# Kernel tuning notes

Measured on AMD Instinct MI355X. Metric: run time of the kernel, lower is better.

The kernel has to match this reference:

```python
import jax, jax.numpy as jnp
import numpy as np

NHEAD = 8
TOP_K = 2


def layernorm(x, g, b, eps=1e-5):
    m = x.mean(-1, keepdims=True)
    v = x.var(-1, keepdims=True)
    return (x - m) * jax.lax.rsqrt(v + eps) * g + b


def causal_conv(x, w, b, dil):
    # x: [N, C, L], w: [O, I, K] (torch layout), left-pad for causality
    pad = (w.shape[-1] - 1) * dil
    y = jax.lax.conv_general_dilated(x, w, (1,), [(pad, 0)], rhs_dilation=(dil,),
                                     dimension_numbers=('NCH', 'OIH', 'NCH'))
    return y + b[None, :, None]


def sinusoidal_pe(L, d):
    pos = jnp.arange(L, dtype=jnp.float32)[:, None]
    div = jnp.exp(jnp.arange(0, d, 2, dtype=jnp.float32) * (-np.log(10000.0) / d))
    pe = jnp.zeros((L, d), jnp.float32)
    pe = pe.at[:, 0::2].set(jnp.sin(pos * div))
    pe = pe.at[:, 1::2].set(jnp.cos(pos * div))
    return pe


def _forward(x, sensor_mask, enc_proj_w, enc_proj_b, tcn_w1, tcn_b1, tcn_w2, tcn_b2,
             enc_norm_g, enc_norm_b, pool_proj_w, pool_proj_b, pos_inter,
             t_wq, t_bq, t_wk, t_bk, t_wv, t_bv, t_wo, t_bo,
             t_ln1_g, t_ln1_b, t_ln2_g, t_ln2_b,
             t_ff1_w, t_ff1_b, t_ff2_w, t_ff2_b, t_out_g, t_out_b,
             exp_w1, exp_b1, exp_w2, exp_b2,
             gate_f_w, gate_f_b, gate_fail_w, gate_fail_b, gate_rca_w, gate_rca_b,
             pred_w, pred_b, fail_w, fail_b, rca_w, rca_b):
    B, L, M = x.shape
    P = enc_proj_w.shape[1]
    D = pool_proj_w.shape[1]
    O = exp_w2.shape[-1]
    # mask sensors, grab last value per sensor (globally standardized)
    xm = jnp.transpose(x, (0, 2, 1)) * sensor_mask[:, :, None]        # [B, M, L]
    last_val = xm[:, :, -1]                                           # [B, M]
    seqs = xm.reshape(B * M, L, 1)
    # per-sensor TCN encoder
    h = seqs @ enc_proj_w + enc_proj_b                                # [BM, L, P]
    h = h + sinusoidal_pe(L, P)[None]
    h = jnp.transpose(h, (0, 2, 1))                                   # [BM, P, L]
    for i in range(tcn_w1.shape[0]):
        dil = 2 ** i
        out = jax.nn.relu(causal_conv(h, tcn_w1[i], tcn_b1[i], dil))
        out = jax.nn.relu(causal_conv(out, tcn_w2[i], tcn_b2[i], dil))
        h = jax.nn.relu(out + h)                                      # channels equal -> identity residual
    h = layernorm(jnp.transpose(h, (0, 2, 1)), enc_norm_g, enc_norm_b)  # [BM, L, T]
    feats = h.reshape(B, M, L, -1) * sensor_mask[:, :, None, None]
    pooled = feats.mean(axis=2)                                       # [B, M, T]
    t = pooled @ pool_proj_w + pool_proj_b                            # [B, M, D]
    # inter-sensor transformer (pre-LN), key padding mask where sensor_mask==0
    t = t + pos_inter[:, :M, :]
    bias = jnp.where(sensor_mask == 0, -1e9, 0.0)[:, None, None, :]   # [B,1,1,M]
    dh = D // NHEAD
    for l in range(t_wq.shape[0]):
        y = layernorm(t, t_ln1_g[l], t_ln1_b[l])
        q = (y @ t_wq[l] + t_bq[l]).reshape(B, M, NHEAD, dh)
        k = (y @ t_wk[l] + t_bk[l]).reshape(B, M, NHEAD, dh)
        v = (y @ t_wv[l] + t_bv[l]).reshape(B, M, NHEAD, dh)
        s = jnp.einsum('bqhd,bkhd->bhqk', q, k) / jnp.sqrt(jnp.float32(dh)) + bias
        a = jax.nn.softmax(s, axis=-1)
        o = jnp.einsum('bhqk,bkhd->bqhd', a, v).reshape(B, M, D) @ t_wo[l] + t_bo[l]
        t = t + o
        y2 = layernorm(t, t_ln2_g[l], t_ln2_b[l])
        t = t + jax.nn.relu(y2 @ t_ff1_w[l] + t_ff1_b[l]) @ t_ff2_w[l] + t_ff2_b[l]
    ctx = layernorm(t, t_out_g, t_out_b) * sensor_mask[:, :, None]    # [B, M, D]
    # global context: masked mean + masked max over valid sensors
    cnt = jnp.maximum(sensor_mask.sum(1, keepdims=True), 1.0)
    mean_ctx = ctx.sum(1) / cnt                                       # [B, D]
    max_ctx = jnp.where(sensor_mask[:, :, None] > 0, ctx, -1e9).max(1)
    g = jnp.concatenate([mean_ctx, max_ctx], -1)                      # [B, 2D]

    def moe(x_exp, gate_in, gw, gb):
        logits = gate_in @ gw + gb                                    # [N, E]
        vals, idx = jax.lax.top_k(logits, TOP_K)
        w = jax.nn.softmax(vals, -1)
        hh = jax.nn.relu(jnp.einsum('nd,edh->neh', x_exp, exp_w1) + exp_b1)
        allo = jnp.einsum('neh,eho->neo', hh, exp_w2) + exp_b2        # [N, E, O]
        sel = jnp.take_along_axis(allo, idx[..., None], axis=1)
        return (sel * w[..., None]).sum(1)                            # [N, O]

    y_f = moe(g, g, gate_f_w, gate_f_b)                               # [B, O]
    y_fail = moe(g, g, gate_fail_w, gate_fail_b)
    tok = ctx.reshape(B * M, D)
    exp_in_rca = jnp.concatenate(
        [tok, jnp.broadcast_to(mean_ctx[:, None, :], (B, M, D)).reshape(B * M, D)], -1)
    y_rca = moe(exp_in_rca, tok, gate_rca_w, gate_rca_b).reshape(B, M, O)
    # heads
    pred_in = jnp.concatenate([pooled, ctx, jnp.broadcast_to(y_f[:, None, :], (B, M, O))], -1)
    pred = pred_in @ pred_w + pred_b + last_val[..., None]            # [B, M, PH]
    fail_out = y_fail @ fail_w + fail_b                               # [B, FH]
    rca_in = jnp.concatenate([pooled, ctx, y_rca], -1)
    rca_out = (rca_in @ rca_w + rca_b)[..., 0]                        # [B, M]
    return jnp.concatenate([pred.reshape(B, -1), fail_out, rca_out], axis=1)


def setup_inputs() -> dict:
    key = jax.random.key(0)
    ks = iter(jax.random.split(key, 64))
    nrm = lambda shape, s=0.05: jax.random.normal(next(ks), shape, jnp.float32) * s
    B, L, M = 16, 512, 32
    P, T, D, E, EH, O = 64, 64, 128, 16, 512, 128
    NL, LEV, K = 2, 4, 3
    return dict(
        x=jax.random.normal(next(ks), (B, L, M), jnp.float32),
        sensor_mask=jax.random.randint(next(ks), (B, M), 0, 2).astype(jnp.float32),
        enc_proj_w=nrm((1, P)), enc_proj_b=jnp.zeros((P,)),
        tcn_w1=nrm((LEV, P, P, K)), tcn_b1=jnp.zeros((LEV, P)),
        tcn_w2=nrm((LEV, P, P, K)), tcn_b2=jnp.zeros((LEV, P)),
        enc_norm_g=jnp.ones((T,)), enc_norm_b=jnp.zeros((T,)),
        pool_proj_w=nrm((T, D)), pool_proj_b=jnp.zeros((D,)),
        pos_inter=nrm((1, M, D), 0.02),
        t_wq=nrm((NL, D, D)), t_bq=jnp.zeros((NL, D)),
        t_wk=nrm((NL, D, D)), t_bk=jnp.zeros((NL, D)),
        t_wv=nrm((NL, D, D)), t_bv=jnp.zeros((NL, D)),
        t_wo=nrm((NL, D, D)), t_bo=jnp.zeros((NL, D)),
        t_ln1_g=jnp.ones((NL, D)), t_ln1_b=jnp.zeros((NL, D)),
        t_ln2_g=jnp.ones((NL, D)), t_ln2_b=jnp.zeros((NL, D)),
        t_ff1_w=nrm((NL, D, 2 * D)), t_ff1_b=jnp.zeros((NL, 2 * D)),
        t_ff2_w=nrm((NL, 2 * D, D)), t_ff2_b=jnp.zeros((NL, D)),
        t_out_g=jnp.ones((D,)), t_out_b=jnp.zeros((D,)),
        exp_w1=nrm((E, 2 * D, EH)), exp_b1=jnp.zeros((E, EH)),
        exp_w2=nrm((E, EH, O)), exp_b2=jnp.zeros((E, O)),
        gate_f_w=nrm((2 * D, E)), gate_f_b=jnp.zeros((E,)),
        gate_fail_w=nrm((2 * D, E)), gate_fail_b=jnp.zeros((E,)),
        gate_rca_w=nrm((D, E)), gate_rca_b=jnp.zeros((E,)),
        pred_w=nrm((T + D + O, 3)), pred_b=jnp.zeros((3,)),
        fail_w=nrm((O, 3)), fail_b=jnp.zeros((3,)),
        rca_w=nrm((T + D + O, 1)), rca_b=jnp.zeros((1,)),
    )


def reference(x, sensor_mask, enc_proj_w, enc_proj_b, tcn_w1, tcn_b1, tcn_w2, tcn_b2,
              enc_norm_g, enc_norm_b, pool_proj_w, pool_proj_b, pos_inter,
              t_wq, t_bq, t_wk, t_bk, t_wv, t_bv, t_wo, t_bo,
              t_ln1_g, t_ln1_b, t_ln2_g, t_ln2_b,
              t_ff1_w, t_ff1_b, t_ff2_w, t_ff2_b, t_out_g, t_out_b,
              exp_w1, exp_b1, exp_w2, exp_b2,
              gate_f_w, gate_f_b, gate_fail_w, gate_fail_b, gate_rca_w, gate_rca_b,
              pred_w, pred_b, fail_w, fail_b, rca_w, rca_b):
    return _forward(x, sensor_mask, enc_proj_w, enc_proj_b, tcn_w1, tcn_b1, tcn_w2, tcn_b2,
                    enc_norm_g, enc_norm_b, pool_proj_w, pool_proj_b, pos_inter,
                    t_wq, t_bq, t_wk, t_bk, t_wv, t_bv, t_wo, t_bo,
                    t_ln1_g, t_ln1_b, t_ln2_g, t_ln2_b,
                    t_ff1_w, t_ff1_b, t_ff2_w, t_ff2_b, t_out_g, t_out_b,
                    exp_w1, exp_b1, exp_w2, exp_b2,
                    gate_f_w, gate_f_b, gate_fail_w, gate_fail_b, gate_rca_w, gate_rca_b,
                    pred_w, pred_b, fail_w, fail_b, rca_w, rca_b)
```

## Files before the change

### kernel.cpp

```cpp
#include <hip/hip_runtime.h>
#include <hip/hip_bf16.h>

#define B_   16
#define L_   512
#define M_   32
#define P_   64
#define D_   128
#define NH_  8
#define NL_  2
#define E_   16
#define EH_  512
#define O_   128

#define CH2   256
#define HALO  60
#define PADF  16
#define ROWS2 336
#define LDW   64

typedef short  bf16x8 __attribute__((ext_vector_type(8)));
typedef float  f32x4  __attribute__((ext_vector_type(4)));
typedef unsigned short us4 __attribute__((ext_vector_type(4)));
typedef unsigned short us8 __attribute__((ext_vector_type(8)));

__device__ __forceinline__ float bf2f(unsigned short h) {
  unsigned u = ((unsigned)h) << 16; float f; __builtin_memcpy(&f, &u, 4); return f;
}
__device__ __forceinline__ unsigned short f2bf(float f) {
  unsigned u; __builtin_memcpy(&u, &f, 4);
  u += 0x7fffu + ((u >> 16) & 1);
  return (unsigned short)(u >> 16);
}
__device__ __forceinline__ int swz(int row, int col_us) {
  return row * LDW + (col_us ^ ((row & 7) << 3));
}

#define XFW_PPW   0
#define XFW_QKVO  8192
#define XFW_F1    139264
#define XFW_F2    204800

__global__ __launch_bounds__(256) void prep_kernel(
    const float* __restrict__ ppw,
    const float* __restrict__ twq, const float* __restrict__ twk,
    const float* __restrict__ twv, const float* __restrict__ two,
    const float* __restrict__ f1w, const float* __restrict__ f2w,
    const float* __restrict__ ew1, const float* __restrict__ ew2,
    const float* __restrict__ tw1, const float* __restrict__ tw2,
    unsigned short* __restrict__ xfw, unsigned short* __restrict__ w1t,
    unsigned short* __restrict__ w2t, unsigned short* __restrict__ wpack,
    float* __restrict__ peT) {
  const int b = blockIdx.x;
  const int tid = threadIdx.x;
  if (b < 834) {
    __shared__ float tl[64][65];
    const float* src; unsigned short* dst; int R, C, tr, tc;
    if (b < 2) {
      src = ppw; dst = xfw + XFW_PPW; R = 64; C = 128; tr = 0; tc = b;
    } else if (b < 34) {
      int t = b - 2; int lg = t >> 2; int l = lg >> 2, gem = lg & 3;
      int tt = t & 3; tr = tt >> 1; tc = tt & 1;
      const float* s4 = (gem == 0) ? twq : (gem == 1) ? twk : (gem == 2) ? twv : two;
      src = s4 + l * 16384; dst = xfw + XFW_QKVO + l * 65536 + gem * 16384; R = 128; C = 128;
    } else if (b < 50) {
      int t = b - 34; int l = t >> 3; int tt = t & 7; tr = tt >> 2; tc = tt & 3;
      src = f1w + l * 32768; dst = xfw + XFW_F1 + l * 32768; R = 128; C = 256;
    } else if (b < 66) {
      int t = b - 50; int l = t >> 3; int tt = t & 7; tr = tt >> 1; tc = tt & 1;
      src = f2w + l * 32768; dst = xfw + XFW_F2 + l * 32768; R = 256; C = 128;
    } else if (b < 578) {
      int t = b - 66; int e = t >> 5; int tt = t & 31; tr = tt >> 3; tc = tt & 7;
      src = ew1 + e * 131072; dst = w1t + e * 131072; R = 256; C = 512;
    } else {
      int t = b - 578; int e = t >> 4; int tt = t & 15; tr = tt >> 1; tc = tt & 1;
      src = ew2 + e * 65536; dst = w2t + e * 65536; R = 512; C = 128;
    }
    for (int i = tid; i < 4096; i += 256) {
      int r = i >> 6, c = i & 63;
      tl[r][c] = src[(tr * 64 + r) * C + tc * 64 + c];
    }
    __syncthreads();
    for (int i = tid; i < 4096; i += 256) {
      int c = i >> 6, r = i & 63;
      dst[(tc * 64 + c) * R + tr * 64 + r] = f2bf(tl[r][c]);
    }
  } else if (b < 840) {
    int base = (b - 834) * 16384;
    for (int q = tid; q < 16384; q += 256) {
      int i = base + q;
      int c = i & 63, o = (i >> 6) & 63, tlc = i >> 12;
      int t = tlc % 3, lc = tlc / 3, lvl = lc >> 1;
      const float* src = (lc & 1) ? tw2 : tw1;
      wpack[i] = f2bf(src[lvl * 12288 + o * 192 + c * 3 + t]);
    }
  } else {
    int base = (b - 840) * 16384;
    for (int q = tid; q < 16384; q += 256) {
      int j = base + q; int ll = j >> 6, c = j & 63;
      float dv = expf(-0.14391157f * (float)(c & ~1));
      float ang = (float)ll * dv;
      peT[j] = (c & 1) ? cosf(ang) : sinf(ang);
    }
  }
}

template <int DIL, bool RES>
__device__ __forceinline__ void conv_mfma(const unsigned short* __restrict__ IN,
                                          unsigned short* __restrict__ OUT,
                                          const unsigned short* __restrict__ Wt,
                                          const float* __restrict__ bias, bool zh) {
  const int tid  = threadIdx.x;
  const int wid  = tid >> 6;
  const int lane = tid & 63;
  const int fr   = lane & 15;
  const int g    = lane >> 4;
  const int ot0  = (wid & 1) * 2;
  const int ng   = wid >> 1;

  bf16x8 Af[2][6];
#pragma unroll
  for (int oo = 0; oo < 2; ++oo)
#pragma unroll
    for (int t = 0; t < 3; ++t)
#pragma unroll
      for (int kh = 0; kh < 2; ++kh) {
        int wr = t * 64 + (ot0 + oo) * 16 + fr;
        Af[oo][t * 2 + kh] = *(const bf16x8*)(Wt + swz(wr, kh * 32 + g * 8));
      }
  float bv[2][4];
#pragma unroll
  for (int oo = 0; oo < 2; ++oo)
#pragma unroll
    for (int j = 0; j < 4; ++j) bv[oo][j] = bias[(ot0 + oo) * 16 + g * 4 + j];

#pragma unroll
  for (int k = 0; k < 3; ++k) {
    const int nt = ng + k * 8;
    if (nt < 20) {
      const int rb = PADF + nt * 16 + fr;
      bf16x8 Bf[6];
#pragma unroll
      for (int t = 0; t < 3; ++t) {
        int r = rb + (t - 2) * DIL;
#pragma unroll
        for (int kh = 0; kh < 2; ++kh)
          Bf[t * 2 + kh] = *(const bf16x8*)(IN + swz(r, kh * 32 + g * 8));
      }
      f32x4 acc[2];
#pragma unroll
      for (int oo = 0; oo < 2; ++oo) {
        f32x4 a; a[0] = bv[oo][0]; a[1] = bv[oo][1]; a[2] = bv[oo][2]; a[3] = bv[oo][3];
        acc[oo] = a;
      }
#pragma unroll
      for (int f = 0; f < 6; ++f)
#pragma unroll
        for (int oo = 0; oo < 2; ++oo)
          acc[oo] = __builtin_amdgcn_mfma_f32_16x16x32_bf16(Af[oo][f], Bf[f], acc[oo], 0, 0, 0);

      const float zm = (zh && rb < PADF + HALO) ? 0.f : 1.f;
#pragma unroll
      for (int oo = 0; oo < 2; ++oo) {
        unsigned short* op = OUT + swz(rb, (ot0 + oo) * 16 + g * 4);
        us4 old;
        if (RES) old = *(const us4*)op;
        us4 st;
#pragma unroll
        for (int j = 0; j < 4; ++j) {
          float v = fmaxf(acc[oo][j], 0.f);
          if (RES) v = fmaxf(v + bf2f(old[j]), 0.f);
          st[j] = f2bf(v * zm);
        }
        *(us4*)op = st;
      }
    }
  }
}

__global__ __launch_bounds__(1024) void tcn_kernel(
    const float* __restrict__ x, const float* __restrict__ mask,
    const float* __restrict__ pw, const float* __restrict__ pb,
    const unsigned short* __restrict__ wpack,
    const float* __restrict__ b1, const float* __restrict__ b2,
    const float* __restrict__ peT,
    const float* __restrict__ lng, const float* __restrict__ lnb,
    float* __restrict__ psum2) {
  extern __shared__ unsigned short smu[];
  unsigned short* A  = smu;
  unsigned short* Bq = A + ROWS2 * LDW;
  unsigned short* W0 = Bq + ROWS2 * LDW;
  unsigned short* W1 = W0 + 192 * LDW;
  float* fbase = (float*)(W1 + 192 * LDW);
  float* xr   = fbase;
  float* pwpb = fbase + 336;
  float* mst  = fbase;
  float* pp   = fbase + 512;

  const int bx = blockIdx.x;
  const int seq = bx & 511;
  const int chunk = bx >> 9;
  const int b = seq >> 5;
  const int m = seq & 31;
  if (mask[b * M_ + m] == 0.0f) return;
  const int tid = threadIdx.x;
  const bool zh = (chunk == 0);
  const int lbase = chunk * CH2 - HALO;

  float4 wreg[2];
#define WLOAD(li)                                                               \
  { wreg[0] = *(const float4*)(wpack + (li) * 12288 + (tid >> 3) * 64 + (tid & 7) * 8); \
    if (tid < 512)                                                              \
      wreg[1] = *(const float4*)(wpack + (li) * 12288 + ((tid >> 3) + 128) * 64 + (tid & 7) * 8); }
#define WSTORE(buf)                                                             \
  { *(float4*)((buf) + swz(tid >> 3, (tid & 7) * 8)) = wreg[0];                 \
    if (tid < 512)                                                              \
      *(float4*)((buf) + swz((tid >> 3) + 128, (tid & 7) * 8)) = wreg[1]; }

  WLOAD(0);
  if (tid < 64)       pwpb[tid] = pw[tid];
  else if (tid < 128) pwpb[tid] = pb[tid - 64];
  if (tid < ROWS2) {
    int w = tid - PADF, l = lbase + w;
    float xv = 0.f;
    if (w >= 0 && w < CH2 + HALO && l >= 0 && l < L_) xv = x[(b * L_ + l) * M_ + m];
    xr[tid] = xv;
  }
  __syncthreads();

  for (int idx = tid; idx < ROWS2 * 8; idx += 1024) {
    int r = idx >> 3, c0 = (idx & 7) * 8;
    int w = r - PADF, l = lbase + w;
    us8 st;
    if (w >= 0 && w < CH2 + HALO && l >= 0 && l < L_) {
      float xv = xr[r];
      const float4* pe4 = (const float4*)(peT + l * 64 + c0);
      float4 pa = pe4[0], pc = pe4[1];
      float pe[8] = {pa.x, pa.y, pa.z, pa.w, pc.x, pc.y, pc.z, pc.w};
#pragma unroll
      for (int j = 0; j < 8; ++j) {
        int c = c0 + j;
        st[j] = f2bf(fmaf(xv, pwpb[c], pwpb[64 + c]) + pe[j]);
      }
    } else {
#pragma unroll
      for (int j = 0; j < 8; ++j) st[j] = 0;
    }
    *(us8*)(A + swz(r, c0)) = st;
  }
  for (int idx = tid; idx < PADF * LDW; idx += 1024) Bq[idx] = 0;
  WSTORE(W0); WLOAD(1);
  __syncthreads();

  conv_mfma<1, false>(A, Bq, W0, b1 + 0,   zh); WSTORE(W1); WLOAD(2); __syncthreads();
  conv_mfma<1, true >(Bq, A, W1, b2 + 0,   zh); WSTORE(W0); WLOAD(3); __syncthreads();
  conv_mfma<2, false>(A, Bq, W0, b1 + 64,  zh); WSTORE(W1); WLOAD(4); __syncthreads();
  conv_mfma<2, true >(Bq, A, W1, b2 + 64,  zh); WSTORE(W0); WLOAD(5); __syncthreads();
  conv_mfma<4, false>(A, Bq, W0, b1 + 128, zh); WSTORE(W1); WLOAD(6); __syncthreads();
  conv_mfma<4, true >(Bq, A, W1, b2 + 128, zh); WSTORE(W0); WLOAD(7); __syncthreads();
  conv_mfma<8, false>(A, Bq, W0, b1 + 192, zh); WSTORE(W1);           __syncthreads();
  conv_mfma<8, true >(Bq, A, W1, b2 + 192, zh);                       __syncthreads();
#undef WLOAD
#undef WSTORE

  if (tid < CH2) {
    int r = PADF + HALO + tid;
    float s = 0.f, ss = 0.f;
#pragma unroll
    for (int c0 = 0; c0 < 64; c0 += 8) {
      bf16x8 vv = *(const bf16x8*)(A + swz(r, c0));
#pragma unroll
      for (int j = 0; j < 8; ++j) { float v = bf2f((unsigned short)vv[j]); s += v; ss += v * v; }
    }
    float mu = s * 0.015625f;
    float var = fmaxf(ss * 0.015625f - mu * mu, 0.0f);
    mst[tid] = mu;
    mst[CH2 + tid] = rsqrtf(var + 1e-5f);
  }
  __syncthreads();
  {
    int p = tid & 63, q = tid >> 6;
    float accp = 0.f;
    int r0 = PADF + HALO + q * 16;
    for (int r = r0; r < r0 + 16; ++r)
      accp += (bf2f(A[swz(r, p)]) - mst[r - PADF - HALO]) * mst[CH2 + r - PADF - HALO];
    pp[tid] = accp;
  }
  __syncthreads();
  if (tid < 64) {
    float acc = 0.f;
#pragma unroll
    for (int q = 0; q < 16; ++q) acc += pp[q * 64 + tid];
    psum2[chunk * 32768 + seq * 64 + tid] = lng[tid] * acc + 256.0f * lnb[tid];
  }
}

__device__ __forceinline__ void ln_sums(const float* __restrict__ In, float* mst, float* scr) {
  const int t = threadIdx.x;
  if (t < 256) {
    int mm = t >> 3, sg = t & 7;
    const float* ip = In + mm * 132 + sg * 16;
    float s = 0, ss = 0;
#pragma unroll
    for (int j = 0; j < 16; ++j) { float v = ip[j]; s += v; ss += v * v; }
    scr[t] = s; scr[256 + t] = ss;
  }
  __syncthreads();
  if (t < 32) {
    float s = 0, ss = 0;
#pragma unroll
    for (int k = 0; k < 8; ++k) { s += scr[t * 8 + k]; ss += scr[256 + t * 8 + k]; }
    float mu = s * 0.0078125f;
    float var = fmaxf(ss * 0.0078125f - mu * mu, 0.f);
    mst[t] = mu;
    mst[32 + t] = rsqrtf(var + 1e-5f);
  }
  __syncthreads();
}

__device__ __forceinline__ void ln_bf(const float* __restrict__ In, unsigned short* __restrict__ Out,
                                      const float* __restrict__ g, const float* __restrict__ b,
                                      float* mst, float* scr) {
  ln_sums(In, mst, scr);
  for (int idx = threadIdx.x; idx < 4096; idx += 512) {
    int mm = idx >> 7, j = idx & 127;
    Out[mm * 136 + j] = f2bf((In[mm * 132 + j] - mst[mm]) * mst[32 + mm] * g[j] + b[j]);
  }
  __syncthreads();
}

__device__ __forceinline__ void ln_f32(const float* __restrict__ In, float* __restrict__ Out,
                                       const float* __restrict__ g, const float* __restrict__ b,
                                       float* mst, float* scr) {
  ln_sums(In, mst, scr);
  for (int idx = threadIdx.x; idx < 4096; idx += 512) {
    int mm = idx >> 7, j = idx & 127;
    Out[mm * 132 + j] = (In[mm * 132 + j] - mst[mm]) * mst[32 + mm] * g[j] + b[j];
  }
  __syncthreads();
}

__global__ __launch_bounds__(512) void xf_kernel(
    const float* __restrict__ psum2, const float* __restrict__ mask,
    const unsigned short* __restrict__ xfw,
    const float* __restrict__ ppb, const float* __restrict__ pos,
    const float* __restrict__ bq, const float* __restrict__ bk,
    const float* __restrict__ bv, const float* __restrict__ bo,
    const float* __restrict__ l1g, const float* __restrict__ l1b,
    const float* __restrict__ l2g, const float* __restrict__ l2b,
    const float* __restrict__ f1b, const float* __restrict__ f2b,
    const float* __restrict__ og_, const float* __restrict__ ob_,
    const float* __restrict__ gfw, const float* __restrict__ gfb,
    const float* __restrict__ glw, const float* __restrict__ glb,
    const float* __restrict__ grw, const float* __restrict__ grb,
    float* __restrict__ pooledws, float* __restrict__ ctxws,
    float* __restrict__ gwt, int* __restrict__ ecnt, int* __restrict__ elist,
    unsigned short* __restrict__ xbf) {
  extern __shared__ float sm[];
  float* T    = sm;
  float* QKV  = T + 4224;
  float* S    = QKV + 12672;
  float* scr  = S + 8448;
  float* mst  = scr + 512;
  float* mkv  = mst + 64;
  unsigned short* Ybf = (unsigned short*)(mkv + 32);
  unsigned short* Yb2 = Ybf + 32 * 136;
  unsigned short* FFH = Yb2 + 32 * 136;
  const int b = blockIdx.x;
  const int tid = threadIdx.x;
  const int wid = tid >> 6;
  const int lane = tid & 63;
  const int fr = lane & 15;
  const int g = lane >> 4;

  if (tid < 32) mkv[tid] = mask[b * 32 + tid];
  for (int idx = tid; idx < 2048; idx += 512) {
    int mm = idx >> 6, p = idx & 63;
    const float* p4 = psum2 + (b * 32 + mm) * 64 + p;
    float v = (p4[0] + p4[32768]) * mask[b * 32 + mm] * (1.0f / 512.0f);
    pooledws[(b * 32 + mm) * 64 + p] = v;
    Ybf[mm * 136 + p] = f2bf(v);
  }
  __syncthreads();

  {
    int mt = wid >> 2;
    bf16x8 Af[2];
#pragma unroll
    for (int kf = 0; kf < 2; ++kf)
      Af[kf] = *(const bf16x8*)(Ybf + (mt * 16 + fr) * 136 + kf * 32 + g * 8);
#pragma unroll
    for (int i = 0; i < 2; ++i) {
      int nt = (wid & 3) * 2 + i;
      const unsigned short* bp = xfw + XFW_PPW + (nt * 16 + fr) * 64;
      f32x4 acc = {0.f, 0.f, 0.f, 0.f};
#pragma unroll
      for (int kf = 0; kf < 2; ++kf)
        acc = __builtin_amdgcn_mfma_f32_16x16x32_bf16(Af[kf], *(const bf16x8*)(bp + kf * 32 + g * 8), acc, 0, 0, 0);
      int n = nt * 16 + fr;
      float bb = ppb[n];
#pragma unroll
      for (int j = 0; j < 4; ++j) {
        int m = mt * 16 + g * 4 + j;
        T[m * 132 + n] = acc[j] + bb + pos[m * 128 + n];
      }
    }
  }
  __syncthreads();

  for (int l = 0; l < NL_; ++l) {
    ln_bf(T, Ybf, l1g + l * 128, l1b + l * 128, mst, scr);
#pragma unroll
    for (int i = 0; i < 6; ++i) {
      int tt = wid * 6 + i;
      int gem = tt >> 4, r = tt & 15, mt = r >> 3, nt = r & 7;
      const unsigned short* wT = xfw + XFW_QKVO + l * 65536 + gem * 16384;
      const float* bias = (gem == 0) ? bq : (gem == 1) ? bk : bv;
      bf16x8 Afr[4];
#pragma unroll
      for (int kf = 0; kf < 4; ++kf)
        Afr[kf] = *(const bf16x8*)(Ybf + (mt * 16 + fr) * 136 + kf * 32 + g * 8);
      const unsigned short* bp = wT + (nt * 16 + fr) * 128;
      f32x4 acc = {0.f, 0.f, 0.f, 0.f};
#pragma unroll
      for (int kf = 0; kf < 4; ++kf)
        acc = __builtin_amdgcn_mfma_f32_16x16x32_bf16(Afr[kf], *(const bf16x8*)(bp + kf * 32 + g * 8), acc, 0, 0, 0);
      int n = nt * 16 + fr;
      float bb = bias[l * 128 + n];
#pragma unroll
      for (int j = 0; j < 4; ++j)
        QKV[(mt * 16 + g * 4 + j) * 396 + gem * 132 + n] = acc[j] + bb;
    }
    __syncthreads();
    for (int idx = tid; idx < 8192; idx += 512) {
      int h = idx >> 10, rem = idx & 1023, mm = rem >> 5, n = rem & 31;
      const float* qp = QKV + mm * 396 + h * 16;
      const float* kp = QKV + n * 396 + 132 + h * 16;
      float a = 0;
#pragma unroll
      for (int d = 0; d < 16; ++d) a = fmaf(qp[d], kp[d], a);
      a *= 0.25f;
      if (mkv[n] == 0.0f) a -= 1e9f;
      S[h * 1056 + mm * 33 + n] = a;
    }
    __syncthreads();
    if (tid < 256) {
      float* sr = S + (tid >> 5) * 1056 + (tid & 31) * 33;
      float mx = sr[0];
      for (int n = 1; n < 32; ++n) mx = fmaxf(mx, sr[n]);
      float sum = 0;
      for (int n = 0; n < 32; ++n) { float e = __expf(sr[n] - mx); sr[n] = e; sum += e; }
      float inv = 1.0f / sum;
      for (int n = 0; n < 32; ++n) sr[n] *= inv;
    }
    __syncthreads();
    for (int idx = tid; idx < 4096; idx += 512) {
      int mm = idx >> 7, jd = idx & 127, h = jd >> 4, d = jd & 15;
      const float* sp = S + h * 1056 + mm * 33;
      const float* vp = QKV + 264 + h * 16 + d;
      float a = 0;
#pragma unroll 8
      for (int n = 0; n < 32; ++n) a = fmaf(sp[n], vp[n * 396], a);
      Yb2[mm * 136 + jd] = f2bf(a);
    }
    __syncthreads();
    {
      int mt = wid >> 2;
      bf16x8 Aw[4];
#pragma unroll
      for (int kf = 0; kf < 4; ++kf)
        Aw[kf] = *(const bf16x8*)(Yb2 + (mt * 16 + fr) * 136 + kf * 32 + g * 8);
#pragma unroll
      for (int i = 0; i < 2; ++i) {
        int nt = (wid & 3) * 2 + i;
        const unsigned short* bp = xfw + XFW_QKVO + l * 65536 + 3 * 16384 + (nt * 16 + fr) * 128;
        f32x4 acc = {0.f, 0.f, 0.f, 0.f};
#pragma unroll
        for (int kf = 0; kf < 4; ++kf)
          acc = __builtin_amdgcn_mfma_f32_16x16x32_bf16(Aw[kf], *(const bf16x8*)(bp + kf * 32 + g * 8), acc, 0, 0, 0);
        int n = nt * 16 + fr;
        float bb = bo[l * 128 + n];
#pragma unroll
        for (int j = 0; j < 4; ++j)
          T[(mt * 16 + g * 4 + j) * 132 + n] += acc[j] + bb;
      }
    }
    __syncthreads();
    ln_bf(T, Ybf, l2g + l * 128, l2b + l * 128, mst, scr);
    {
      int mt = wid >> 2;
      bf16x8 Aff[4];
#pragma unroll
      for (int kf = 0; kf < 4; ++kf)
        Aff[kf] = *(const bf16x8*)(Ybf + (mt * 16 + fr) * 136 + kf * 32 + g * 8);
#pragma unroll
      for (int i = 0; i < 4; ++i) {
        int tt = wid * 4 + i;
        int nt = tt & 15;
        const unsigned short* bp = xfw + XFW_F1 + l * 32768 + (nt * 16 + fr) * 128;
        f32x4 acc = {0.f, 0.f, 0.f, 0.f};
#pragma unroll
        for (int kf = 0; kf < 4; ++kf)
          acc = __builtin_amdgcn_mfma_f32_16x16x32_bf16(Aff[kf], *(const bf16x8*)(bp + kf * 32 + g * 8), acc, 0, 0, 0);
        int n = nt * 16 + fr;
        float bb = f1b[l * 256 + n];
#pragma unroll
        for (int j = 0; j < 4; ++j)
          FFH[(mt * 16 + g * 4 + j) * 264 + n] = f2bf(fmaxf(acc[j] + bb, 0.f));
      }
    }
    __syncthreads();
    {
      int mt = wid >> 2;
      bf16x8 Af2[8];
#pragma unroll
      for (int kf = 0; kf < 8; ++kf)
        Af2[kf] = *(const bf16x8*)(FFH + (mt * 16 + fr) * 264 + kf * 32 + g * 8);
#pragma unroll
      for (int i = 0; i < 2; ++i) {
        int nt = (wid & 3) * 2 + i;
        const unsigned short* bp = xfw + XFW_F2 + l * 32768 + (nt * 16 + fr) * 256;
        f32x4 acc = {0.f, 0.f, 0.f, 0.f};
#pragma unroll
        for (int kf = 0; kf < 8; ++kf)
          acc = __builtin_amdgcn_mfma_f32_16x16x32_bf16(Af2[kf], *(const bf16x8*)(bp + kf * 32 + g * 8), acc, 0, 0, 0);
        int n = nt * 16 + fr;
        float bb = f2b[l * 128 + n];
#pragma unroll
        for (int j = 0; j < 4; ++j)
          T[(mt * 16 + g * 4 + j) * 132 + n] += acc[j] + bb;
      }
    }
    __syncthreads();
  }

  ln_f32(T, S, og_, ob_, mst, scr);
  for (int idx = tid; idx < 4096; idx += 512) {
    int mm = idx >> 7, j = idx & 127;
    float c = S[mm * 132 + j] * mkv[mm];
    S[mm * 132 + j] = c;
    ctxws[(b * 32 + mm) * 128 + j] = c;
  }
  __syncthreads();
  if (tid < 128) {
    float cnt = 0;
    for (int mm = 0; mm < 32; ++mm) cnt += mkv[mm];
    cnt = fmaxf(cnt, 1.0f);
    float s = 0, mx = -1e9f;
    for (int mm = 0; mm < 32; ++mm) {
      float v = S[mm * 132 + tid];
      s += v;
      if (mkv[mm] > 0.0f) mx = fmaxf(mx, v);
    }
    scr[tid] = s / cnt;
    scr[128 + tid] = mx;
  }
  __syncthreads();

  float* lg = QKV;
  for (int j = tid; j < 544; j += 512) {
    int lr = j >> 4, e = j & 15;
    float a;
    if (lr == 0) {
      a = gfb[e];
      for (int d = 0; d < 256; ++d) a = fmaf(scr[d], gfw[d * 16 + e], a);
    } else if (lr == 1) {
      a = glb[e];
      for (int d = 0; d < 256; ++d) a = fmaf(scr[d], glw[d * 16 + e], a);
    } else {
      int mm = lr - 2;
      a = grb[e];
      for (int d = 0; d < 128; ++d) a = fmaf(S[mm * 132 + d], grw[d * 16 + e], a);
    }
    lg[lr * 16 + e] = a;
  }
  __syncthreads();
  if (tid < 34) {
    const float* lgr = lg + tid * 16;
    int i0 = 0; float v0 = lgr[0];
    for (int e = 1; e < 16; ++e) if (lgr[e] > v0) { v0 = lgr[e]; i0 = e; }
    int i1 = (i0 == 0) ? 1 : 0; float v1 = lgr[i1];
    for (int e = 0; e < 16; ++e) if (e != i0 && lgr[e] > v1) { v1 = lgr[e]; i1 = e; }
    float e1 = __expf(v1 - v0);
    float w0 = 1.0f / (1.0f + e1);
    int gr = (tid == 0) ? b : (tid == 1) ? (16 + b) : (32 + b * 32 + (tid - 2));
    gwt[2 * gr] = w0;  gwt[2 * gr + 1] = 1.0f - w0;
    int p0 = atomicAdd(&ecnt[i0], 1); elist[i0 * 544 + p0] = 2 * gr;
    int p1 = atomicAdd(&ecnt[i1], 1); elist[i1 * 544 + p1] = 2 * gr + 1;
  }
  for (int j = tid; j < 34 * 256; j += 512) {
    int lr = j >> 8, d = j & 255;
    float v;
    if (lr < 2) v = scr[d];
    else        v = (d < 128) ? S[(lr - 2) * 132 + d] : scr[d - 128];
    int gr = (lr == 0) ? b : (lr == 1) ? (16 + b) : (32 + b * 32 + (lr - 2));
    xbf[gr * 256 + d] = f2bf(v);
  }
}

__global__ __launch_bounds__(512) void moe_kernel(
    const unsigned short* __restrict__ xbf, const float* __restrict__ gwt,
    const int* __restrict__ elist, const int* __restrict__ ecnt,
    const unsigned short* __restrict__ w1t, const float* __restrict__ eb1,
    const unsigned short* __restrict__ w2t, const float* __restrict__ eb2,
    float* __restrict__ yall) {
  __shared__ unsigned short Xb[16 * 264];
  __shared__ unsigned short Hb[16 * 520];
  __shared__ float wl[16];
  __shared__ int rowl[16];
  const int e = blockIdx.x >> 3;
  const int slot = blockIdx.x & 7;
  const int n = ecnt[e];
  const int ntiles = (n + 15) >> 4;
  const int tid = threadIdx.x;
  const int wid = tid >> 6;
  const int lane = tid & 63;
  const int fr = lane & 15;
  const int g = lane >> 4;

  for (int t = slot; t < ntiles; t += 8) {
    if (tid < 16) {
      int idx = t * 16 + tid;
      int id = (idx < n) ? elist[e * 544 + idx] : -1;
      rowl[tid] = (id >= 0) ? (id >> 1) : -1;
      wl[tid] = (id >= 0) ? gwt[id] : 0.f;
    }
    __syncthreads();
    for (int i = tid; i < 512; i += 512) {
      int r = i >> 5, c8 = (i & 31) * 8;
      int row = rowl[r];
      bf16x8 v = {0, 0, 0, 0, 0, 0, 0, 0};
      if (row >= 0) v = *(const bf16x8*)(xbf + row * 256 + c8);
      *(bf16x8*)(Xb + r * 264 + c8) = v;
    }
    __syncthreads();
    bf16x8 Af[8];
#pragma unroll
    for (int kf = 0; kf < 8; ++kf)
      Af[kf] = *(const bf16x8*)(Xb + fr * 264 + kf * 32 + g * 8);
#pragma unroll
    for (int ntl = 0; ntl < 4; ++ntl) {
      int nt = wid * 4 + ntl;
      const unsigned short* bp = w1t + (e * 512 + nt * 16 + fr) * 256;
      f32x4 acc = {0.f, 0.f, 0.f, 0.f};
#pragma unroll
      for (int kf = 0; kf < 8; ++kf)
        acc = __builtin_amdgcn_mfma_f32_16x16x32_bf16(Af[kf], *(const bf16x8*)(bp + kf * 32 + g * 8), acc, 0, 0, 0);
      int h = nt * 16 + fr;
      float b1v = eb1[e * 512 + h];
#pragma unroll
      for (int j = 0; j < 4; ++j)
        Hb[(g * 4 + j) * 520 + h] = f2bf(fmaxf(acc[j] + b1v, 0.f));
    }
    __syncthreads();
    {
      const unsigned short* bp = w2t + (e * 128 + wid * 16 + fr) * 512;
      f32x4 acc = {0.f, 0.f, 0.f, 0.f};
#pragma unroll
      for (int kf = 0; kf < 16; ++kf) {
        bf16x8 Ah = *(const bf16x8*)(Hb + fr * 520 + kf * 32 + g * 8);
        acc = __builtin_amdgcn_mfma_f32_16x16x32_bf16(Ah, *(const bf16x8*)(bp + kf * 32 + g * 8), acc, 0, 0, 0);
      }
      int o = wid * 16 + fr;
      float b2v = eb2[e * 128 + o];
#pragma unroll
      for (int j = 0; j < 4; ++j) {
        int r = g * 4 + j;
        int row = rowl[r];
        if (row >= 0) atomicAdd(&yall[row * 128 + o], wl[r] * (acc[j] + b2v));
      }
    }
    __syncthreads();
  }
}

__global__ __launch_bounds__(192) void heads_kernel(
    const float* __restrict__ x, const float* __restrict__ mask,
    const float* __restrict__ pooledws, const float* __restrict__ ctxws,
    const float* __restrict__ yf, const float* __restrict__ yfail, const float* __restrict__ yrca,
    const float* __restrict__ pw, const float* __restrict__ pb,
    const float* __restrict__ fw, const float* __restrict__ fb,
    const float* __restrict__ rw, const float* __restrict__ rb,
    float* __restrict__ out) {
  __shared__ float yfb[128];
  int b = blockIdx.x, t = threadIdx.x;
  if (t < 128) yfb[t] = yf[b * 128 + t];
  __syncthreads();
  if (t < 96) {
    int mm = t / 3, o = t - mm * 3;
    int s = b * 32 + mm;
    float a = pb[o];
    const float* pl = pooledws + s * 64;
    for (int i = 0; i < 64; ++i) a = fmaf(pl[i], pw[i * 3 + o], a);
    const float* cx = ctxws + s * 128;
    for (int i = 0; i < 128; ++i) a = fmaf(cx[i], pw[(64 + i) * 3 + o], a);
    for (int i = 0; i < 128; ++i) a = fmaf(yfb[i], pw[(192 + i) * 3 + o], a);
    a += x[(b * 512 + 511) * 32 + mm] * mask[b * 32 + mm];
    out[b * 131 + t] = a;
  } else if (t < 99) {
    int o = t - 96;
    float a = fb[o];
    const float* yl = yfail + b * 128;
    for (int i = 0; i < 128; ++i) a = fmaf(yl[i], fw[i * 3 + o], a);
    out[b * 131 + 96 + o] = a;
  } else if (t < 131) {
    int mm = t - 99;
    int s = b * 32 + mm;
    float a = rb[0];
    const float* pl = pooledws + s * 64;
    for (int i = 0; i < 64; ++i) a = fmaf(pl[i], rw[i], a);
    const float* cx = ctxws + s * 128;
    for (int i = 0; i < 128; ++i) a = fmaf(cx[i], rw[64 + i], a);
    const float* yr = yrca + s * 128;
    for (int i = 0; i < 128; ++i) a = fmaf(yr[i], rw[192 + i], a);
    out[b * 131 + 99 + mm] = a;
  }
}

extern "C" void kernel_launch(void* const* d_in, const int* in_sizes, int n_in,
                              void* d_out, int out_size, void* d_ws, size_t ws_size,
                              hipStream_t stream) {
  (void)in_sizes; (void)n_in; (void)out_size; (void)ws_size;
  const float* x    = (const float*)d_in[0];
  const float* msk  = (const float*)d_in[1];
  const float* epw  = (const float*)d_in[2];
  const float* epb  = (const float*)d_in[3];
  const float* tw1  = (const float*)d_in[4];
  const float* tb1  = (const float*)d_in[5];
  const float* tw2  = (const float*)d_in[6];
  const float* tb2  = (const float*)d_in[7];
  const float* eng  = (const float*)d_in[8];
  const float* enb  = (const float*)d_in[9];
  const float* ppw  = (const float*)d_in[10];
  const float* ppb  = (const float*)d_in[11];
  const float* pos  = (const float*)d_in[12];
  const float* twq  = (const float*)d_in[13];
  const float* tbq  = (const float*)d_in[14];
  const float* twk  = (const float*)d_in[15];
  const float* tbk  = (const float*)d_in[16];
  const float* twv  = (const float*)d_in[17];
  const float* tbv  = (const float*)d_in[18];
  const float* two  = (const float*)d_in[19];
  const float* tbo  = (const float*)d_in[20];
  const float* l1g  = (const float*)d_in[21];
  const float* l1b  = (const float*)d_in[22];
  const float* l2g  = (const float*)d_in[23];
  const float* l2b  = (const float*)d_in[24];
  const float* f1w  = (const float*)d_in[25];
  const float* f1b  = (const float*)d_in[26];
  const float* f2w  = (const float*)d_in[27];
  const float* f2b  = (const float*)d_in[28];
  const float* tog  = (const float*)d_in[29];
  const float* tob  = (const float*)d_in[30];
  const float* ew1  = (const float*)d_in[31];
  const float* eb1  = (const float*)d_in[32];
  const float* ew2  = (const float*)d_in[33];
  const float* eb2  = (const float*)d_in[34];
  const float* gfw  = (const float*)d_in[35];
  const float* gfb  = (const float*)d_in[36];
  const float* glw  = (const float*)d_in[37];
  const float* glb  = (const float*)d_in[38];
  const float* grw  = (const float*)d_in[39];
  const float* grb  = (const float*)d_in[40];
  const float* prw  = (const float*)d_in[41];
  const float* prb  = (const float*)d_in[42];
  const float* fw   = (const float*)d_in[43];
  const float* fb   = (const float*)d_in[44];
  const float* rw   = (const float*)d_in[45];
  const float* rb   = (const float*)d_in[46];

  float* ws      = (float*)d_ws;
  float* psum2   = ws;
  float* pooledw = psum2 + 65536;
  float* ctxw    = pooledw + 32768;
  float* yall    = ctxw + 65536;
  float* gwt     = yall + 69632;
  int*   ecnt    = (int*)(gwt + 1088);
  int*   elist   = ecnt + 16;
  float* peT     = (float*)(elist + 8704);
  unsigned short* wpack = (unsigned short*)(peT + 32768);
  unsigned short* xfw   = wpack + 98304;
  unsigned short* w1t   = xfw + 270336;
  unsigned short* w2t   = w1t + 2097152;
  unsigned short* xbf   = w2t + 1048576;

  const int tcn_lds = (2 * ROWS2 * LDW + 2 * 192 * LDW) * 2 + 1536 * 4;
  const int xf_lds  = (4224 + 12672 + 8448 + 512 + 64 + 32 + 2176 + 2176 + 4224) * 4;
  hipFuncSetAttribute((const void*)tcn_kernel, hipFuncAttributeMaxDynamicSharedMemorySize, tcn_lds);
  hipFuncSetAttribute((const void*)xf_kernel,  hipFuncAttributeMaxDynamicSharedMemorySize, xf_lds);

  hipMemsetAsync(yall, 0, 69632 * sizeof(float), stream);
  hipMemsetAsync(ecnt, 0, 16 * sizeof(int), stream);

  prep_kernel<<<842, 256, 0, stream>>>(ppw, twq, twk, twv, two, f1w, f2w, ew1, ew2,
                                       tw1, tw2, xfw, w1t, w2t, wpack, peT);
  tcn_kernel<<<1024, 1024, tcn_lds, stream>>>(x, msk, epw, epb, wpack, tb1, tb2, peT,
                                              eng, enb, psum2);
  xf_kernel<<<16, 512, xf_lds, stream>>>(psum2, msk, xfw, ppb, pos,
                                         tbq, tbk, tbv, tbo,
                                         l1g, l1b, l2g, l2b, f1b, f2b,
                                         tog, tob,
                                         gfw, gfb, glw, glb, grw, grb,
                                         pooledw, ctxw, gwt, ecnt, elist, xbf);
  moe_kernel<<<128, 512, 0, stream>>>(xbf, gwt, elist, ecnt, w1t, eb1, w2t, eb2, yall);
  heads_kernel<<<16, 192, 0, stream>>>(x, msk, pooledw, ctxw,
                                       yall, yall + 2048, yall + 4096,
                                       prw, prb, fw, fb, rw, rb, (float*)d_out);
}
```

Baseline: 252.7 us.

## Run transformer kernel with 1024 threads and warp-shuffle layernorm and softmax

The per-batch transformer kernel now launches 1024 threads per block instead of 512, so each wave owns a single MFMA output tile instead of looping over several. LayerNorm switches from two LDS passes with barriers to one pass where 32 lanes per row reduce with shuffles. Attention scores and softmax are fused into a single shuffle-reduced pass, and the PV product is vectorised with float4 loads. The aim is to cut barriers and serial latency in a kernel that only runs 16 blocks, at the cost of more threads, higher register pressure per block and a rebalanced LDS layout.

Result: faster. 241.8 us (-4.3%).

```diff
diff --git a/kernel.cpp b/kernel.cpp
--- a/kernel.cpp
+++ b/kernel.cpp
@@ -294,52 +294,7 @@
   }
 }
 
-__device__ __forceinline__ void ln_sums(const float* __restrict__ In, float* mst, float* scr) {
-  const int t = threadIdx.x;
-  if (t < 256) {
-    int mm = t >> 3, sg = t & 7;
-    const float* ip = In + mm * 132 + sg * 16;
-    float s = 0, ss = 0;
-#pragma unroll
-    for (int j = 0; j < 16; ++j) { float v = ip[j]; s += v; ss += v * v; }
-    scr[t] = s; scr[256 + t] = ss;
-  }
-  __syncthreads();
-  if (t < 32) {
-    float s = 0, ss = 0;
-#pragma unroll
-    for (int k = 0; k < 8; ++k) { s += scr[t * 8 + k]; ss += scr[256 + t * 8 + k]; }
-    float mu = s * 0.0078125f;
-    float var = fmaxf(ss * 0.0078125f - mu * mu, 0.f);
-    mst[t] = mu;
-    mst[32 + t] = rsqrtf(var + 1e-5f);
-  }
-  __syncthreads();
-}
-
-__device__ __forceinline__ void ln_bf(const float* __restrict__ In, unsigned short* __restrict__ Out,
-                                      const float* __restrict__ g, const float* __restrict__ b,
-                                      float* mst, float* scr) {
-  ln_sums(In, mst, scr);
-  for (int idx = threadIdx.x; idx < 4096; idx += 512) {
-    int mm = idx >> 7, j = idx & 127;
-    Out[mm * 136 + j] = f2bf((In[mm * 132 + j] - mst[mm]) * mst[32 + mm] * g[j] + b[j]);
-  }
-  __syncthreads();
-}
-
-__device__ __forceinline__ void ln_f32(const float* __restrict__ In, float* __restrict__ Out,
-                                       const float* __restrict__ g, const float* __restrict__ b,
-                                       float* mst, float* scr) {
-  ln_sums(In, mst, scr);
-  for (int idx = threadIdx.x; idx < 4096; idx += 512) {
-    int mm = idx >> 7, j = idx & 127;
-    Out[mm * 132 + j] = (In[mm * 132 + j] - mst[mm]) * mst[32 + mm] * g[j] + b[j];
-  }
-  __syncthreads();
-}
-
-__global__ __launch_bounds__(512) void xf_kernel(
+__global__ __launch_bounds__(1024) void xf_kernel(
     const float* __restrict__ psum2, const float* __restrict__ mask,
     const unsigned short* __restrict__ xfw,
     const float* __restrict__ ppb, const float* __restrict__ pos,
@@ -359,10 +314,9 @@
   float* T    = sm;
   float* QKV  = T + 4224;
   float* S    = QKV + 12672;
-  float* scr  = S + 8448;
-  float* mst  = scr + 512;
-  float* mkv  = mst + 64;
-  unsigned short* Ybf = (unsigned short*)(mkv + 32);
+  float* gv   = S + 8448;
+  float* mkv  = gv + 512;
+  unsigned short* Ybf = (unsigned short*)(mkv + 64);
   unsigned short* Yb2 = Ybf + 32 * 136;
   unsigned short* FFH = Yb2 + 32 * 136;
   const int b = blockIdx.x;
@@ -371,9 +325,11 @@
   const int lane = tid & 63;
   const int fr = lane & 15;
   const int g = lane >> 4;
+  const int row32 = tid >> 5;
+  const int ln32  = tid & 31;
 
   if (tid < 32) mkv[tid] = mask[b * 32 + tid];
-  for (int idx = tid; idx < 2048; idx += 512) {
+  for (int idx = tid; idx < 2048; idx += 1024) {
     int mm = idx >> 6, p = idx & 63;
     const float* p4 = psum2 + (b * 32 + mm) * 64 + p;
     float v = (p4[0] + p4[32768]) * mask[b * 32 + mm] * (1.0f / 512.0f);
@@ -383,35 +339,50 @@
   __syncthreads();
 
   {
-    int mt = wid >> 2;
+    int mt = wid >> 3, nt = wid & 7;
     bf16x8 Af[2];
 #pragma unroll
     for (int kf = 0; kf < 2; ++kf)
       Af[kf] = *(const bf16x8*)(Ybf + (mt * 16 + fr) * 136 + kf * 32 + g * 8);
-#pragma unroll
-    for (int i = 0; i < 2; ++i) {
-      int nt = (wid & 3) * 2 + i;
-      const unsigned short* bp = xfw + XFW_PPW + (nt * 16 + fr) * 64;
-      f32x4 acc = {0.f, 0.f, 0.f, 0.f};
-#pragma unroll
-      for (int kf = 0; kf < 2; ++kf)
-        acc = __builtin_amdgcn_mfma_f32_16x16x32_bf16(Af[kf], *(const bf16x8*)(bp + kf * 32 + g * 8), acc, 0, 0, 0);
-      int n = nt * 16 + fr;
-      float bb = ppb[n];
-#pragma unroll
-      for (int j = 0; j < 4; ++j) {
-        int m = mt * 16 + g * 4 + j;
-        T[m * 132 + n] = acc[j] + bb + pos[m * 128 + n];
-      }
-    }
-  }
+    const unsigned short* bp = xfw + XFW_PPW + (nt * 16 + fr) * 64;
+    f32x4 acc = {0.f, 0.f, 0.f, 0.f};
+#pragma unroll
+    for (int kf = 0; kf < 2; ++kf)
+      acc = __builtin_amdgcn_mfma_f32_16x16x32_bf16(Af[kf], *(const bf16x8*)(bp + kf * 32 + g * 8), acc, 0, 0, 0);
+    int n = nt * 16 + fr;
+    float bb = ppb[n];
+#pragma unroll
+    for (int j = 0; j < 4; ++j) {
+      int m = mt * 16 + g * 4 + j;
+      T[m * 132 + n] = acc[j] + bb + pos[m * 128 + n];
+    }
+  }
+  __syncthreads();
+
+#define LN_BF(GAMMA, BETA)                                                     \
+  {                                                                            \
+    int mm = row32, j0 = ln32 * 4;                                             \
+    float4 v4 = *(const float4*)(T + mm * 132 + j0);                           \
+    float s = v4.x + v4.y + v4.z + v4.w;                                       \
+    float ss = v4.x * v4.x + v4.y * v4.y + v4.z * v4.z + v4.w * v4.w;          \
+    _Pragma("unroll") for (int mk = 16; mk >= 1; mk >>= 1) {                   \
+      s += __shfl_xor(s, mk); ss += __shfl_xor(ss, mk);                        \
+    }                                                                          \
+    float mu = s * 0.0078125f;                                                 \
+    float rstd = rsqrtf(fmaxf(ss * 0.0078125f - mu * mu, 0.f) + 1e-5f);        \
+    us4 st;                                                                    \
+    float vv[4] = {v4.x, v4.y, v4.z, v4.w};                                    \
+    _Pragma("unroll") for (int j = 0; j < 4; ++j)                              \
+      st[j] = f2bf((vv[j] - mu) * rstd * (GAMMA)[j0 + j] + (BETA)[j0 + j]);    \
+    *(us4*)(Ybf + mm * 136 + j0) = st;                                         \
+  }                                                                            \
   __syncthreads();
 
   for (int l = 0; l < NL_; ++l) {
-    ln_bf(T, Ybf, l1g + l * 128, l1b + l * 128, mst, scr);
-#pragma unroll
-    for (int i = 0; i < 6; ++i) {
-      int tt = wid * 6 + i;
+    LN_BF(l1g + l * 128, l1b + l * 128)
+#pragma unroll
+    for (int i = 0; i < 3; ++i) {
+      int tt = wid * 3 + i;
       int gem = tt >> 4, r = tt & 15, mt = r >> 3, nt = r & 7;
       const unsigned short* wT = xfw + XFW_QKVO + l * 65536 + gem * 16384;
       const float* bias = (gem == 0) ? bq : (gem == 1) ? bk : bv;
@@ -431,114 +402,128 @@
         QKV[(mt * 16 + g * 4 + j) * 396 + gem * 132 + n] = acc[j] + bb;
     }
     __syncthreads();
-    for (int idx = tid; idx < 8192; idx += 512) {
-      int h = idx >> 10, rem = idx & 1023, mm = rem >> 5, n = rem & 31;
-      const float* qp = QKV + mm * 396 + h * 16;
-      const float* kp = QKV + n * 396 + 132 + h * 16;
-      float a = 0;
-#pragma unroll
-      for (int d = 0; d < 16; ++d) a = fmaf(qp[d], kp[d], a);
-      a *= 0.25f;
-      if (mkv[n] == 0.0f) a -= 1e9f;
-      S[h * 1056 + mm * 33 + n] = a;
-    }
-    __syncthreads();
-    if (tid < 256) {
-      float* sr = S + (tid >> 5) * 1056 + (tid & 31) * 33;
-      float mx = sr[0];
-      for (int n = 1; n < 32; ++n) mx = fmaxf(mx, sr[n]);
-      float sum = 0;
-      for (int n = 0; n < 32; ++n) { float e = __expf(sr[n] - mx); sr[n] = e; sum += e; }
-      float inv = 1.0f / sum;
-      for (int n = 0; n < 32; ++n) sr[n] *= inv;
-    }
-    __syncthreads();
-    for (int idx = tid; idx < 4096; idx += 512) {
-      int mm = idx >> 7, jd = idx & 127, h = jd >> 4, d = jd & 15;
+
+    {
+      int n = ln32;
+      float mbias = (mkv[n] == 0.0f) ? -1e9f : 0.f;
+#pragma unroll
+      for (int t = 0; t < 8; ++t) {
+        int task = row32 * 8 + t;
+        int h = task >> 5, mm = task & 31;
+        const float* qp = QKV + mm * 396 + h * 16;
+        const float* kp = QKV + n * 396 + 132 + h * 16;
+        float a = 0;
+#pragma unroll
+        for (int d = 0; d < 16; ++d) a = fmaf(qp[d], kp[d], a);
+        a = a * 0.25f + mbias;
+        float mx = a;
+#pragma unroll
+        for (int mk = 16; mk >= 1; mk >>= 1) mx = fmaxf(mx, __shfl_xor(mx, mk));
+        float e = __expf(a - mx);
+        float sum = e;
+#pragma unroll
+        for (int mk = 16; mk >= 1; mk >>= 1) sum += __shfl_xor(sum, mk);
+        S[h * 1056 + mm * 33 + n] = e / sum;
+      }
+    }
+    __syncthreads();
+
+    {
+      int mm = row32, j0 = ln32 * 4, h = j0 >> 4;
       const float* sp = S + h * 1056 + mm * 33;
-      const float* vp = QKV + 264 + h * 16 + d;
-      float a = 0;
+      f32x4 a = {0.f, 0.f, 0.f, 0.f};
 #pragma unroll 8
-      for (int n = 0; n < 32; ++n) a = fmaf(sp[n], vp[n * 396], a);
-      Yb2[mm * 136 + jd] = f2bf(a);
-    }
-    __syncthreads();
+      for (int n = 0; n < 32; ++n) {
+        float p = sp[n];
+        float4 v4 = *(const float4*)(QKV + n * 396 + 264 + j0);
+        a[0] = fmaf(p, v4.x, a[0]); a[1] = fmaf(p, v4.y, a[1]);
+        a[2] = fmaf(p, v4.z, a[2]); a[3] = fmaf(p, v4.w, a[3]);
+      }
+      us4 st;
+#pragma unroll
+      for (int j = 0; j < 4; ++j) st[j] = f2bf(a[j]);
+      *(us4*)(Yb2 + mm * 136 + j0) = st;
+    }
+    __syncthreads();
+
     {
-      int mt = wid >> 2;
+      int mt = wid >> 3, nt = wid & 7;
       bf16x8 Aw[4];
 #pragma unroll
       for (int kf = 0; kf < 4; ++kf)
         Aw[kf] = *(const bf16x8*)(Yb2 + (mt * 16 + fr) * 136 + kf * 32 + g * 8);
-#pragma unroll
-      for (int i = 0; i < 2; ++i) {
-        int nt = (wid & 3) * 2 + i;
-        const unsigned short* bp = xfw + XFW_QKVO + l * 65536 + 3 * 16384 + (nt * 16 + fr) * 128;
-        f32x4 acc = {0.f, 0.f, 0.f, 0.f};
-#pragma unroll
-        for (int kf = 0; kf < 4; ++kf)
-          acc = __builtin_amdgcn_mfma_f32_16x16x32_bf16(Aw[kf], *(const bf16x8*)(bp + kf * 32 + g * 8), acc, 0, 0, 0);
-        int n = nt * 16 + fr;
-        float bb = bo[l * 128 + n];
-#pragma unroll
-        for (int j = 0; j < 4; ++j)
-          T[(mt * 16 + g * 4 + j) * 132 + n] += acc[j] + bb;
-      }
-    }
-    __syncthreads();
-    ln_bf(T, Ybf, l2g + l * 128, l2b + l * 128, mst, scr);
-    {
-      int mt = wid >> 2;
+      const unsigned short* bp = xfw + XFW_QKVO + l * 65536 + 3 * 16384 + (nt * 16 + fr) * 128;
+      f32x4 acc = {0.f, 0.f, 0.f, 0.f};
+#pragma unroll
+      for (int kf = 0; kf < 4; ++kf)
+        acc = __builtin_amdgcn_mfma_f32_16x16x32_bf16(Aw[kf], *(const bf16x8*)(bp + kf * 32 + g * 8), acc, 0, 0, 0);
+      int n = nt * 16 + fr;
+      float bb = bo[l * 128 + n];
+#pragma unroll
+      for (int j = 0; j < 4; ++j)
+        T[(mt * 16 + g * 4 + j) * 132 + n] += acc[j] + bb;
+    }
+    __syncthreads();
+
+    LN_BF(l2g + l * 128, l2b + l * 128)
+#pragma unroll
+    for (int i = 0; i < 2; ++i) {
+      int tt = wid * 2 + i;
+      int mt = tt >> 4, nt = tt & 15;
       bf16x8 Aff[4];
 #pragma unroll
       for (int kf = 0; kf < 4; ++kf)
         Aff[kf] = *(const bf16x8*)(Ybf + (mt * 16 + fr) * 136 + kf * 32 + g * 8);
-#pragma unroll
-      for (int i = 0; i < 4; ++i) {
-        int tt = wid * 4 + i;
-        int nt = tt & 15;
-        const unsigned short* bp = xfw + XFW_F1 + l * 32768 + (nt * 16 + fr) * 128;
-        f32x4 acc = {0.f, 0.f, 0.f, 0.f};
-#pragma unroll
-        for (int kf = 0; kf < 4; ++kf)
-          acc = __builtin_amdgcn_mfma_f32_16x16x32_bf16(Aff[kf], *(const bf16x8*)(bp + kf * 32 + g * 8), acc, 0, 0, 0);
-        int n = nt * 16 + fr;
-        float bb = f1b[l * 256 + n];
-#pragma unroll
-        for (int j = 0; j < 4; ++j)
-          FFH[(mt * 16 + g * 4 + j) * 264 + n] = f2bf(fmaxf(acc[j] + bb, 0.f));
-      }
+      const unsigned short* bp = xfw + XFW_F1 + l * 32768 + (nt * 16 + fr) * 128;
+      f32x4 acc = {0.f, 0.f, 0.f, 0.f};
+#pragma unroll
+      for (int kf = 0; kf < 4; ++kf)
+        acc = __builtin_amdgcn_mfma_f32_16x16x32_bf16(Aff[kf], *(const bf16x8*)(bp + kf * 32 + g * 8), acc, 0, 0, 0);
+      int n = nt * 16 + fr;
+      float bb = f1b[l * 256 + n];
+#pragma unroll
+      for (int j = 0; j < 4; ++j)
+        FFH[(mt * 16 + g * 4 + j) * 264 + n] = f2bf(fmaxf(acc[j] + bb, 0.f));
     }
     __syncthreads();
     {
-      int mt = wid >> 2;
+      int mt = wid >> 3, nt = wid & 7;
       bf16x8 Af2[8];
 #pragma unroll
       for (int kf = 0; kf < 8; ++kf)
         Af2[kf] = *(const bf16x8*)(FFH + (mt * 16 + fr) * 264 + kf * 32 + g * 8);
-#pragma unroll
-      for (int i = 0; i < 2; ++i) {
-        int nt = (wid & 3) * 2 + i;
-        const unsigned short* bp = xfw + XFW_F2 + l * 32768 + (nt * 16 + fr) * 256;
-        f32x4 acc = {0.f, 0.f, 0.f, 0.f};
-#pragma unroll
-        for (int kf = 0; kf < 8; ++kf)
-          acc = __builtin_amdgcn_mfma_f32_16x16x32_bf16(Af2[kf], *(const bf16x8*)(bp + kf * 32 + g * 8), acc, 0, 0, 0);
-        int n = nt * 16 + fr;
-        float bb = f2b[l * 128 + n];
-#pragma unroll
-        for (int j = 0; j < 4; ++j)
-          T[(mt * 16 + g * 4 + j) * 132 + n] += acc[j] + bb;
-      }
-    }
-    __syncthreads();
-  }
-
-  ln_f32(T, S, og_, ob_, mst, scr);
-  for (int idx = tid; idx < 4096; idx += 512) {
-    int mm = idx >> 7, j = idx & 127;
-    float c = S[mm * 132 + j] * mkv[mm];
-    S[mm * 132 + j] = c;
-    ctxws[(b * 32 + mm) * 128 + j] = c;
+      const unsigned short* bp = xfw + XFW_F2 + l * 32768 + (nt * 16 + fr) * 256;
+      f32x4 acc = {0.f, 0.f, 0.f, 0.f};
+#pragma unroll
+      for (int kf = 0; kf < 8; ++kf)
+        acc = __builtin_amdgcn_mfma_f32_16x16x32_bf16(Af2[kf], *(const bf16x8*)(bp + kf * 32 + g * 8), acc, 0, 0, 0);
+      int n = nt * 16 + fr;
+      float bb = f2b[l * 128 + n];
+#pragma unroll
+      for (int j = 0; j < 4; ++j)
+        T[(mt * 16 + g * 4 + j) * 132 + n] += acc[j] + bb;
+    }
+    __syncthreads();
+  }
+#undef LN_BF
+
+  {
+    int mm = row32, j0 = ln32 * 4;
+    float4 v4 = *(const float4*)(T + mm * 132 + j0);
+    float s = v4.x + v4.y + v4.z + v4.w;
+    float ss = v4.x * v4.x + v4.y * v4.y + v4.z * v4.z + v4.w * v4.w;
+#pragma unroll
+    for (int mk = 16; mk >= 1; mk >>= 1) { s += __shfl_xor(s, mk); ss += __shfl_xor(ss, mk); }
+    float mu = s * 0.0078125f;
+    float rstd = rsqrtf(fmaxf(ss * 0.0078125f - mu * mu, 0.f) + 1e-5f);
+    float mk_ = mkv[mm];
+    float vv[4] = {v4.x, v4.y, v4.z, v4.w};
+#pragma unroll
+    for (int j = 0; j < 4; ++j) {
+      float c = ((vv[j] - mu) * rstd * og_[j0 + j] + ob_[j0 + j]) * mk_;
+      S[mm * 132 + j0 + j] = c;
+      ctxws[(b * 32 + mm) * 128 + j0 + j] = c;
+    }
   }
   __syncthreads();
   if (tid < 128) {
@@ -551,21 +536,21 @@
       s += v;
       if (mkv[mm] > 0.0f) mx = fmaxf(mx, v);
     }
-    scr[tid] = s / cnt;
-    scr[128 + tid] = mx;
+    gv[tid] = s / cnt;
+    gv[128 + tid] = mx;
   }
   __syncthreads();
 
   float* lg = QKV;
-  for (int j = tid; j < 544; j += 512) {
-    int lr = j >> 4, e = j & 15;
+  if (tid < 544) {
+    int lr = tid >> 4, e = tid & 15;
     float a;
     if (lr == 0) {
       a = gfb[e];
-      for (int d = 0; d < 256; ++d) a = fmaf(scr[d], gfw[d * 16 + e], a);
+      for (int d = 0; d < 256; ++d) a = fmaf(gv[d], gfw[d * 16 + e], a);
     } else if (lr == 1) {
       a = glb[e];
-      for (int d = 0; d < 256; ++d) a = fmaf(scr[d], glw[d * 16 + e], a);
+      for (int d = 0; d < 256; ++d) a = fmaf(gv[d], glw[d * 16 + e], a);
     } else {
       int mm = lr - 2;
       a = grb[e];
@@ -587,11 +572,11 @@
     int p0 = atomicAdd(&ecnt[i0], 1); elist[i0 * 544 + p0] = 2 * gr;
     int p1 = atomicAdd(&ecnt[i1], 1); elist[i1 * 544 + p1] = 2 * gr + 1;
   }
-  for (int j = tid; j < 34 * 256; j += 512) {
+  for (int j = tid; j < 34 * 256; j += 1024) {
     int lr = j >> 8, d = j & 255;
     float v;
-    if (lr < 2) v = scr[d];
-    else        v = (d < 128) ? S[(lr - 2) * 132 + d] : scr[d - 128];
+    if (lr < 2) v = gv[d];
+    else        v = (d < 128) ? S[(lr - 2) * 132 + d] : gv[d - 128];
     int gr = (lr == 0) ? b : (lr == 1) ? (16 + b) : (32 + b * 32 + (lr - 2));
     xbf[gr * 256 + d] = f2bf(v);
   }
@@ -784,7 +769,7 @@
   unsigned short* xbf   = w2t + 1048576;
 
   const int tcn_lds = (2 * ROWS2 * LDW + 2 * 192 * LDW) * 2 + 1536 * 4;
-  const int xf_lds  = (4224 + 12672 + 8448 + 512 + 64 + 32 + 2176 + 2176 + 4224) * 4;
+  const int xf_lds  = (4224 + 12672 + 8448 + 512 + 64) * 4 + (2 * 4352 + 8448) * 2;
   hipFuncSetAttribute((const void*)tcn_kernel, hipFuncAttributeMaxDynamicSharedMemorySize, tcn_lds);
   hipFuncSetAttribute((const void*)xf_kernel,  hipFuncAttributeMaxDynamicSharedMemorySize, xf_lds);
 
@@ -795,12 +780,12 @@
                                        tw1, tw2, xfw, w1t, w2t, wpack, peT);
   tcn_kernel<<<1024, 1024, tcn_lds, stream>>>(x, msk, epw, epb, wpack, tb1, tb2, peT,
                                               eng, enb, psum2);
-  xf_kernel<<<16, 512, xf_lds, stream>>>(psum2, msk, xfw, ppb, pos,
-                                         tbq, tbk, tbv, tbo,
-                                         l1g, l1b, l2g, l2b, f1b, f2b,
-                                         tog, tob,
-                                         gfw, gfb, glw, glb, grw, grb,
-                                         pooledw, ctxw, gwt, ecnt, elist, xbf);
+  xf_kernel<<<16, 1024, xf_lds, stream>>>(psum2, msk, xfw, ppb, pos,
+                                          tbq, tbk, tbv, tbo,
+                                          l1g, l1b, l2g, l2b, f1b, f2b,
+                                          tog, tob,
+                                          gfw, gfb, glw, glb, grw, grb,
+                                          pooledw, ctxw, gwt, ecnt, elist, xbf);
   moe_kernel<<<128, 512, 0, stream>>>(xbf, gwt, elist, ecnt, w1t, eb1, w2t, eb2, yall);
   heads_kernel<<<16, 192, 0, stream>>>(x, msk, pooledw, ctxw,
                                        yall, yall + 2048, yall + 4096,
```
